# Optimization experiments

Hardware: AMD Instinct MI355X
Metric: run time of the kernel (lower is better)

Reference implementation:

```python
import jax, jax.numpy as jnp
import numpy as np

B = 8192
DIMS = [1024, 1024, 1024, 1024]  # input, hidden0, hidden1, output
RANK = 64


def _apg_layer(x, Wm, bm, U, V, b, activate):
    # hyper-net (MLP_Layer with no hidden units == single Linear): generates rank*rank weights per sample
    w = (x @ Wm.T + bm).reshape(x.shape[0], RANK, RANK)   # [B, r, r]
    u = x @ U.T                                           # U_matrix: [B, r]
    # (u.unsqueeze(-1) * w).sum(-2) == per-sample matvec
    h = jnp.einsum('br,brs->bs', u, w)                    # [B, r]
    out = h @ V.T + b                                     # V_matrix + static bias: [B, out]
    return jax.nn.relu(out) if activate else out


def setup_inputs() -> dict:
    key = jax.random.key(0)
    ks = jax.random.split(key, 16)
    inp = {"x": jax.random.normal(ks[0], (B, DIMS[0]), dtype=jnp.float32)}
    ki = 1
    for l in range(3):
        din, dout = DIMS[l], DIMS[l + 1]
        inp[f"Wm{l}"] = jax.random.normal(ks[ki], (RANK * RANK, din), dtype=jnp.float32) * (1.0 / np.sqrt(din)); ki += 1
        inp[f"bm{l}"] = jnp.zeros((RANK * RANK,), dtype=jnp.float32)
        inp[f"U{l}"] = jax.random.normal(ks[ki], (RANK, din), dtype=jnp.float32) * (1.0 / np.sqrt(din)); ki += 1
        inp[f"V{l}"] = jax.random.normal(ks[ki], (dout, RANK), dtype=jnp.float32) * (1.0 / np.sqrt(RANK)); ki += 1
        inp[f"b{l}"] = jnp.zeros((dout,), dtype=jnp.float32)
    return inp


def reference(x, Wm0, bm0, U0, V0, b0, Wm1, bm1, U1, V1, b1, Wm2, bm2, U2, V2, b2):
    h = _apg_layer(x, Wm0, bm0, U0, V0, b0, activate=True)   # hidden layer 0 + ReLU
    h = _apg_layer(h, Wm1, bm1, U1, V1, b1, activate=True)   # hidden layer 1 + ReLU
    out = _apg_layer(h, Wm2, bm2, U2, V2, b2, activate=False)  # output layer, no activation
    return out
```

## Files before the change

### kernel.cpp

```cpp
#include <hip/hip_runtime.h>
#include <stdint.h>

typedef short bf16x8_t __attribute__((ext_vector_type(8)));
typedef short bf16x4_t __attribute__((ext_vector_type(4)));
typedef float f32x4_t __attribute__((ext_vector_type(4)));
typedef unsigned short u16x4_t __attribute__((ext_vector_type(4)));
typedef unsigned short u16x8_t __attribute__((ext_vector_type(8)));

#define DEV static __device__ __forceinline__

DEV float bf2f(unsigned short u) {
  union { unsigned int i; float f; } v; v.i = ((unsigned int)u) << 16; return v.f;
}
DEV unsigned short f2bf(float f) {
  union { float f; unsigned int i; } v; v.f = f;
  unsigned int x = v.i;
  unsigned int lsb = (x >> 16) & 1u;
  x += 0x7fffu + lsb;
  return (unsigned short)(x >> 16);
}

struct CvtSeg {
  const float* src[3];
  unsigned short* dst[3];
  int bstart[4];
};

DEV void cvt_block(const CvtSeg& cs, int vb, int tid) {
  int seg = (vb >= cs.bstart[1] ? 1 : 0) + (vb >= cs.bstart[2] ? 1 : 0);
  int local = (vb - cs.bstart[seg]) * 256 + tid;
  float4 v = ((const float4*)cs.src[seg])[local];
  u16x4_t o = { f2bf(v.x), f2bf(v.y), f2bf(v.z), f2bf(v.w) };
  *(u16x4_t*)&cs.dst[seg][local * 4] = o;
}

__global__ __launch_bounds__(256) void k_cvt(CvtSeg cs) {
  cvt_block(cs, blockIdx.x, threadIdx.x);
}

__global__ __launch_bounds__(256, 2) void xu_fused(
    const float* __restrict__ x,
    const unsigned short* __restrict__ U0,
    unsigned short* __restrict__ xb,
    unsigned short* __restrict__ u_out) {
  __shared__ unsigned short tlds[4 * 16 * 72];
  __shared__ float upart[4 * 16 * 68];

  const int tid = threadIdx.x;
  const int lane = tid & 63;
  const int w = tid >> 6;
  const int fr = lane & 15;
  const int quad = lane >> 4;
  const int rowBase = blockIdx.x * 16;

  unsigned short* tl = &tlds[w * 16 * 72];
  const int m2 = lane >> 2;
  const int kc = (lane & 3) * 16;

  f32x4_t uacc[4];
#pragma unroll
  for (int n = 0; n < 4; n++) uacc[n] = f32x4_t{0.f, 0.f, 0.f, 0.f};

  for (int it = 0; it < 4; ++it) {
    const int cb = w * 256 + it * 64;

    {
      const float* xp = x + (size_t)(rowBase + m2) * 1024 + cb + kc;
      float4 v0 = *(const float4*)(xp);
      float4 v1 = *(const float4*)(xp + 4);
      float4 v2 = *(const float4*)(xp + 8);
      float4 v3 = *(const float4*)(xp + 12);
      u16x8_t o0 = { f2bf(v0.x), f2bf(v0.y), f2bf(v0.z), f2bf(v0.w),
                     f2bf(v1.x), f2bf(v1.y), f2bf(v1.z), f2bf(v1.w) };
      u16x8_t o1 = { f2bf(v2.x), f2bf(v2.y), f2bf(v2.z), f2bf(v2.w),
                     f2bf(v3.x), f2bf(v3.y), f2bf(v3.z), f2bf(v3.w) };
      *(u16x8_t*)&tl[m2 * 72 + kc] = o0;
      *(u16x8_t*)&tl[m2 * 72 + kc + 8] = o1;
      unsigned short* xo = xb + (size_t)(rowBase + m2) * 1024 + cb + kc;
      *(u16x8_t*)xo = o0;
      *(u16x8_t*)(xo + 8) = o1;
    }

#pragma unroll
    for (int ks = 0; ks < 2; ++ks) {
      bf16x8_t at = *(const bf16x8_t*)&tl[fr * 72 + ks * 32 + quad * 8];
#pragma unroll
      for (int n = 0; n < 4; n++) {
        bf16x8_t bu = *(const bf16x8_t*)&U0[(size_t)(n * 16 + fr) * 1024 + cb +
                                            ks * 32 + quad * 8];
        uacc[n] = __builtin_amdgcn_mfma_f32_16x16x32_bf16(at, bu, uacc[n], 0, 0, 0);
      }
    }
  }

  {
    float* up = &upart[w * 16 * 68];
#pragma unroll
    for (int n = 0; n < 4; n++)
#pragma unroll
      for (int r = 0; r < 4; r++)
        up[(quad * 4 + r) * 68 + n * 16 + fr] = uacc[n][r];
  }
  __syncthreads();
  {
    int m = tid >> 4;
    int c0 = (tid & 15) * 4;
    f32x4_t s = {0.f, 0.f, 0.f, 0.f};
#pragma unroll
    for (int wv = 0; wv < 4; wv++)
      s += *(const f32x4_t*)&upart[wv * 16 * 68 + m * 68 + c0];
    u16x4_t o = { f2bf(s[0]), f2bf(s[1]), f2bf(s[2]), f2bf(s[3]) };
    *(u16x4_t*)&u_out[(size_t)(rowBase + m) * 64 + c0] = o;
  }
}

__global__ __launch_bounds__(256, 2) void k_hyper(
    const unsigned short* __restrict__ A,
    const unsigned short* __restrict__ Wmb,
    const unsigned short* __restrict__ ug,
    const float* __restrict__ bm,
    unsigned short* __restrict__ h_out,
    CvtSeg cs) {
  __shared__ unsigned short smem[16384];

  if (blockIdx.x >= 2048) {
    cvt_block(cs, blockIdx.x - 2048, threadIdx.x);
    return;
  }

  unsigned short* As = smem;
  unsigned short* Bs = smem + 8192;
  const int K = 1024;

  const int tid = threadIdx.x;
  const int lane = tid & 63;
  const int w = tid >> 6;
  const int wrow0 = (w & 1) * 64;
  const int wcol0 = (w >> 1) * 64;
  const int bx = blockIdx.x & 31;
  const int by = blockIdx.x >> 5;
  const int rowBase = by * 128;
  const int colBase = bx * 128;

  const int rl = lane >> 3;
  const int kbg = (lane & 7) ^ rl;
  const int fr = lane & 15;
  const int quad = lane >> 4;

  f32x4_t acc[4][4];
#pragma unroll
  for (int i = 0; i < 4; i++)
#pragma unroll
    for (int j = 0; j < 4; j++) acc[i][j] = f32x4_t{0.f, 0.f, 0.f, 0.f};

  for (int kt = 0; kt < K; kt += 64) {
    __syncthreads();
#pragma unroll
    for (int jj = 0; jj < 4; ++jj) {
      int tr = w * 32 + jj * 8 + rl;
      int ct = colBase + tr;
      int pr = ((ct & 63) << 6) | (ct >> 6);
      const unsigned short* ga = A + (size_t)(rowBase + tr) * K + kt + kbg * 8;
      const unsigned short* gb = Wmb + (size_t)pr * K + kt + kbg * 8;
      __builtin_amdgcn_global_load_lds(
          (const __attribute__((address_space(1))) void*)ga,
          (__attribute__((address_space(3))) void*)&As[(w * 32 + jj * 8) * 64],
          16, 0, 0);
      __builtin_amdgcn_global_load_lds(
          (const __attribute__((address_space(1))) void*)gb,
          (__attribute__((address_space(3))) void*)&Bs[(w * 32 + jj * 8) * 64],
          16, 0, 0);
    }
    __syncthreads();

#pragma unroll
    for (int ks = 0; ks < 2; ++ks) {
      bf16x8_t a[4], b[4];
#pragma unroll
      for (int i = 0; i < 4; i++) {
        int m = wrow0 + i * 16 + fr;
        int slot = (ks * 4 + quad) ^ (m & 7);
        a[i] = *(const bf16x8_t*)&As[m * 64 + slot * 8];
      }
#pragma unroll
      for (int j = 0; j < 4; j++) {
        int n = wcol0 + j * 16 + fr;
        int slot = (ks * 4 + quad) ^ (n & 7);
        b[j] = *(const bf16x8_t*)&Bs[n * 64 + slot * 8];
      }
#pragma unroll
      for (int i = 0; i < 4; i++)
#pragma unroll
        for (int j = 0; j < 4; j++)
          acc[i][j] = __builtin_amdgcn_mfma_f32_16x16x32_bf16(a[i], b[j],
                                                              acc[i][j], 0, 0, 0);
    }
  }

  __syncthreads();

  {
    int row = tid >> 1;
    int c0 = (tid & 1) * 32;
    const unsigned short* up = ug + (size_t)(rowBase + row) * 64 + c0;
    bf16x8_t v0 = *(const bf16x8_t*)(up);
    bf16x8_t v1 = *(const bf16x8_t*)(up + 8);
    bf16x8_t v2 = *(const bf16x8_t*)(up + 16);
    bf16x8_t v3 = *(const bf16x8_t*)(up + 24);
#pragma unroll
    for (int m = 0; m < 8; m++) {
      smem[(c0 + m) * 136 + row] = (unsigned short)v0[m];
      smem[(c0 + 8 + m) * 136 + row] = (unsigned short)v1[m];
      smem[(c0 + 16 + m) * 136 + row] = (unsigned short)v2[m];
      smem[(c0 + 24 + m) * 136 + row] = (unsigned short)v3[m];
    }
  }
  __syncthreads();

  const int s = bx * 2 + (w >> 1);
  float bmv[4];
#pragma unroll
  for (int j = 0; j < 4; j++) bmv[j] = bm[(j * 16 + fr) * 64 + s];

#pragma unroll
  for (int i = 0; i < 4; i++) {
    int row0 = wrow0 + i * 16 + quad * 4;
    bf16x4_t uv[4];
#pragma unroll
    for (int j = 0; j < 4; j++)
      uv[j] = *(const bf16x4_t*)&smem[(j * 16 + fr) * 136 + row0];
#pragma unroll
    for (int r = 0; r < 4; r++) {
      float p = 0.f;
#pragma unroll
      for (int j = 0; j < 4; j++)
        p += bf2f((unsigned short)uv[j][r]) * (acc[i][j][r] + bmv[j]);
      p += __shfl_xor(p, 1, 64);
      p += __shfl_xor(p, 2, 64);
      p += __shfl_xor(p, 4, 64);
      p += __shfl_xor(p, 8, 64);
      if (fr == 0)
        h_out[(size_t)(rowBase + row0 + r) * 64 + s] = f2bf(p);
    }
  }
}

__global__ __launch_bounds__(256, 2) void vu_fused(
    const unsigned short* __restrict__ h,
    const unsigned short* __restrict__ Vb,
    const float* __restrict__ bias,
    const unsigned short* __restrict__ Un,
    unsigned short* __restrict__ act,
    unsigned short* __restrict__ u_out) {
  __shared__ unsigned short tlds[4 * 16 * 72];
  __shared__ float upart[4 * 16 * 68];

  const int tid = threadIdx.x;
  const int lane = tid & 63;
  const int w = tid >> 6;
  const int fr = lane & 15;
  const int quad = lane >> 4;
  const int rowBase = blockIdx.x * 16;

  unsigned short* tl = &tlds[w * 16 * 72];

  bf16x8_t ah0 = *(const bf16x8_t*)&h[(size_t)(rowBase + fr) * 64 + quad * 8];
  bf16x8_t ah1 = *(const bf16x8_t*)&h[(size_t)(rowBase + fr) * 64 + 32 + quad * 8];

  f32x4_t uacc[4];
#pragma unroll
  for (int n = 0; n < 4; n++) uacc[n] = f32x4_t{0.f, 0.f, 0.f, 0.f};

  for (int it = 0; it < 4; ++it) {
    const int cb = w * 256 + it * 64;

    f32x4_t tacc[4];
#pragma unroll
    for (int nt = 0; nt < 4; nt++) {
      const unsigned short* vrow = Vb + (size_t)(cb + nt * 16 + fr) * 64;
      bf16x8_t b0 = *(const bf16x8_t*)&vrow[quad * 8];
      bf16x8_t b1 = *(const bf16x8_t*)&vrow[32 + quad * 8];
      f32x4_t z = {0.f, 0.f, 0.f, 0.f};
      z = __builtin_amdgcn_mfma_f32_16x16x32_bf16(ah0, b0, z, 0, 0, 0);
      tacc[nt] = __builtin_amdgcn_mfma_f32_16x16x32_bf16(ah1, b1, z, 0, 0, 0);
    }

#pragma unroll
    for (int nt = 0; nt < 4; nt++) {
      float bv = bias[cb + nt * 16 + fr];
#pragma unroll
      for (int r = 0; r < 4; r++) {
        float v = tacc[nt][r] + bv;
        v = v > 0.f ? v : 0.f;
        tl[(quad * 4 + r) * 72 + nt * 16 + fr] = f2bf(v);
      }
    }

    {
      int m2 = lane >> 2;
      int kc = (lane & 3) * 16;
      bf16x8_t t0 = *(const bf16x8_t*)&tl[m2 * 72 + kc];
      bf16x8_t t1 = *(const bf16x8_t*)&tl[m2 * 72 + kc + 8];
      unsigned short* ap = act + (size_t)(rowBase + m2) * 1024 + cb + kc;
      *(bf16x8_t*)ap = t0;
      *(bf16x8_t*)(ap + 8) = t1;
    }

#pragma unroll
    for (int ks = 0; ks < 2; ++ks) {
      bf16x8_t at = *(const bf16x8_t*)&tl[fr * 72 + ks * 32 + quad * 8];
#pragma unroll
      for (int n = 0; n < 4; n++) {
        bf16x8_t bu = *(const bf16x8_t*)&Un[(size_t)(n * 16 + fr) * 1024 + cb +
                                            ks * 32 + quad * 8];
        uacc[n] = __builtin_amdgcn_mfma_f32_16x16x32_bf16(at, bu, uacc[n], 0, 0, 0);
      }
    }
  }

  {
    float* up = &upart[w * 16 * 68];
#pragma unroll
    for (int n = 0; n < 4; n++)
#pragma unroll
      for (int r = 0; r < 4; r++)
        up[(quad * 4 + r) * 68 + n * 16 + fr] = uacc[n][r];
  }
  __syncthreads();
  {
    int m = tid >> 4;
    int c0 = (tid & 15) * 4;
    f32x4_t s = {0.f, 0.f, 0.f, 0.f};
#pragma unroll
    for (int wv = 0; wv < 4; wv++)
      s += *(const f32x4_t*)&upart[wv * 16 * 68 + m * 68 + c0];
    u16x4_t o = { f2bf(s[0]), f2bf(s[1]), f2bf(s[2]), f2bf(s[3]) };
    *(u16x4_t*)&u_out[(size_t)(rowBase + m) * 64 + c0] = o;
  }
}

__global__ __launch_bounds__(256, 2) void k_final(
    const unsigned short* __restrict__ A, const unsigned short* __restrict__ B,
    const float* __restrict__ bias, float* __restrict__ Cout) {
  __shared__ unsigned short As[128 * 64];
  __shared__ unsigned short Bs[128 * 64];

  const int tid = threadIdx.x;
  const int lane = tid & 63;
  const int w = tid >> 6;
  const int wrow0 = (w & 1) * 64;
  const int wcol0 = (w >> 1) * 64;
  const int rowBase = blockIdx.y * 128;
  const int colBase = blockIdx.x * 128;

  const int rl = lane >> 3;
  const int kbg = (lane & 7) ^ rl;
  const int fr = lane & 15;
  const int quad = lane >> 4;

  f32x4_t acc[4][4];
#pragma unroll
  for (int i = 0; i < 4; i++)
#pragma unroll
    for (int j = 0; j < 4; j++) acc[i][j] = f32x4_t{0.f, 0.f, 0.f, 0.f};

  __syncthreads();
#pragma unroll
  for (int jj = 0; jj < 4; ++jj) {
    int tr = w * 32 + jj * 8 + rl;
    const unsigned short* ga = A + (size_t)(rowBase + tr) * 64 + kbg * 8;
    const unsigned short* gb = B + (size_t)(colBase + tr) * 64 + kbg * 8;
    __builtin_amdgcn_global_load_lds(
        (const __attribute__((address_space(1))) void*)ga,
        (__attribute__((address_space(3))) void*)&As[(w * 32 + jj * 8) * 64],
        16, 0, 0);
    __builtin_amdgcn_global_load_lds(
        (const __attribute__((address_space(1))) void*)gb,
        (__attribute__((address_space(3))) void*)&Bs[(w * 32 + jj * 8) * 64],
        16, 0, 0);
  }
  __syncthreads();

#pragma unroll
  for (int ks = 0; ks < 2; ++ks) {
    bf16x8_t a[4], b[4];
#pragma unroll
    for (int i = 0; i < 4; i++) {
      int m = wrow0 + i * 16 + fr;
      int slot = (ks * 4 + quad) ^ (m & 7);
      a[i] = *(const bf16x8_t*)&As[m * 64 + slot * 8];
    }
#pragma unroll
    for (int j = 0; j < 4; j++) {
      int n = wcol0 + j * 16 + fr;
      int slot = (ks * 4 + quad) ^ (n & 7);
      b[j] = *(const bf16x8_t*)&Bs[n * 64 + slot * 8];
    }
#pragma unroll
    for (int i = 0; i < 4; i++)
#pragma unroll
      for (int j = 0; j < 4; j++)
        acc[i][j] = __builtin_amdgcn_mfma_f32_16x16x32_bf16(a[i], b[j],
                                                            acc[i][j], 0, 0, 0);
  }

#pragma unroll
  for (int j = 0; j < 4; j++) {
    int col = colBase + wcol0 + j * 16 + fr;
    float bv = bias[col];
#pragma unroll
    for (int i = 0; i < 4; i++) {
#pragma unroll
      for (int r = 0; r < 4; r++) {
        int row = rowBase + wrow0 + i * 16 + quad * 4 + r;
        Cout[(size_t)row * 1024 + col] = acc[i][j][r] + bv;
      }
    }
  }
}

extern "C" void kernel_launch(void* const* d_in, const int* in_sizes, int n_in,
                              void* d_out, int out_size, void* d_ws,
                              size_t ws_size, hipStream_t stream) {
  const float* x = (const float*)d_in[0];
  const float* Wm[3] = {(const float*)d_in[1], (const float*)d_in[6], (const float*)d_in[11]};
  const float* bm[3] = {(const float*)d_in[2], (const float*)d_in[7], (const float*)d_in[12]};
  const float* U[3]  = {(const float*)d_in[3], (const float*)d_in[8], (const float*)d_in[13]};
  const float* V[3]  = {(const float*)d_in[4], (const float*)d_in[9], (const float*)d_in[14]};
  const float* bs[3] = {(const float*)d_in[5], (const float*)d_in[10], (const float*)d_in[15]};

  char* p = (char*)d_ws;
  unsigned short* xb = (unsigned short*)p;  p += 8192UL * 1024 * 2;
  unsigned short* act = (unsigned short*)p; p += 8192UL * 1024 * 2;
  unsigned short* Wmb[3];
  for (int l = 0; l < 3; l++) { Wmb[l] = (unsigned short*)p; p += 4096UL * 1024 * 2; }
  unsigned short* Ub[3];
  for (int l = 0; l < 3; l++) { Ub[l] = (unsigned short*)p; p += 64UL * 1024 * 2; }
  unsigned short* Vb[3];
  for (int l = 0; l < 3; l++) { Vb[l] = (unsigned short*)p; p += 1024UL * 64 * 2; }
  unsigned short* hb = (unsigned short*)p;  p += 8192UL * 64 * 2;
  unsigned short* ug = (unsigned short*)p;  p += 8192UL * 64 * 2;

  CvtSeg c0;
  c0.src[0] = Wm[0]; c0.dst[0] = Wmb[0];
  c0.src[1] = U[0];  c0.dst[1] = Ub[0];
  c0.src[2] = U[0];  c0.dst[2] = Ub[0];
  c0.bstart[0] = 0; c0.bstart[1] = 4096; c0.bstart[2] = 4160; c0.bstart[3] = 4160;
  k_cvt<<<4160, 256, 0, stream>>>(c0);

  xu_fused<<<512, 256, 0, stream>>>(x, Ub[0], xb, ug);

  CvtSeg ch[3];
  ch[0].src[0] = Wm[1]; ch[0].dst[0] = Wmb[1];
  ch[0].src[1] = U[1];  ch[0].dst[1] = Ub[1];
  ch[0].src[2] = V[0];  ch[0].dst[2] = Vb[0];
  ch[0].bstart[0] = 0; ch[0].bstart[1] = 4096; ch[0].bstart[2] = 4160; ch[0].bstart[3] = 4224;
  ch[1].src[0] = Wm[2]; ch[1].dst[0] = Wmb[2];
  ch[1].src[1] = U[2];  ch[1].dst[1] = Ub[2];
  ch[1].src[2] = V[1];  ch[1].dst[2] = Vb[1];
  ch[1].bstart[0] = 0; ch[1].bstart[1] = 4096; ch[1].bstart[2] = 4160; ch[1].bstart[3] = 4224;
  ch[2].src[0] = V[2]; ch[2].dst[0] = Vb[2];
  ch[2].src[1] = V[2]; ch[2].dst[1] = Vb[2];
  ch[2].src[2] = V[2]; ch[2].dst[2] = Vb[2];
  ch[2].bstart[0] = 0; ch[2].bstart[1] = 64; ch[2].bstart[2] = 64; ch[2].bstart[3] = 64;

  const int hyperGrid[3] = {2048 + 4224, 2048 + 4224, 2048 + 64};

  const unsigned short* cur = xb;
  for (int l = 0; l < 3; l++) {
    k_hyper<<<hyperGrid[l], 256, 0, stream>>>(cur, Wmb[l], ug, bm[l], hb, ch[l]);
    if (l < 2) {
      vu_fused<<<512, 256, 0, stream>>>(hb, Vb[l], bs[l], Ub[l + 1], act, ug);
      cur = act;
    } else {
      k_final<<<dim3(8, 64), 256, 0, stream>>>(hb, Vb[2], bs[2], (float*)d_out);
    }
  }
}
```

Before: 413.8 us.

## Rewrite hyper GEMM with 256x256 tiles, 8 waves, 4-stage LDS pipeline

The hypernetwork GEMM kernel moves from 128x128 tiles with 4 waves and single-buffered K=64 steps to 256x256 tiles with 8 waves (512 threads). It uses a 4-slot ring of K=32 LDS buffers filled by direct global-to-LDS loads issued two steps ahead, with explicit waitcnt, barriers and s_setprio around the MFMA bursts. The aim is to hide global load latency and raise data reuse per tile. The cost is 128KB of LDS per block and far fewer blocks (512), which limits occupancy. The fused conversion blocks are resized to 512 threads to match.

```diff
diff --git a/kernel.cpp b/kernel.cpp
--- a/kernel.cpp
+++ b/kernel.cpp
@@ -29,6 +29,14 @@
 DEV void cvt_block(const CvtSeg& cs, int vb, int tid) {
   int seg = (vb >= cs.bstart[1] ? 1 : 0) + (vb >= cs.bstart[2] ? 1 : 0);
   int local = (vb - cs.bstart[seg]) * 256 + tid;
+  float4 v = ((const float4*)cs.src[seg])[local];
+  u16x4_t o = { f2bf(v.x), f2bf(v.y), f2bf(v.z), f2bf(v.w) };
+  *(u16x4_t*)&cs.dst[seg][local * 4] = o;
+}
+
+DEV void cvt_block512(const CvtSeg& cs, int vb, int tid) {
+  int seg = (vb >= cs.bstart[1] ? 1 : 0) + (vb >= cs.bstart[2] ? 1 : 0);
+  int local = (vb - cs.bstart[seg]) * 512 + tid;
   float4 v = ((const float4*)cs.src[seg])[local];
   u16x4_t o = { f2bf(v.x), f2bf(v.y), f2bf(v.z), f2bf(v.w) };
   *(u16x4_t*)&cs.dst[seg][local * 4] = o;
@@ -114,87 +122,113 @@
   }
 }
 
-__global__ __launch_bounds__(256, 2) void k_hyper(
+#define GLD(gp, lp)                                              \
+  __builtin_amdgcn_global_load_lds(                              \
+      (const __attribute__((address_space(1))) void*)(gp),       \
+      (__attribute__((address_space(3))) void*)(lp), 16, 0, 0)
+
+__global__ __launch_bounds__(512, 2) void k_hyper(
     const unsigned short* __restrict__ A,
     const unsigned short* __restrict__ Wmb,
     const unsigned short* __restrict__ ug,
     const float* __restrict__ bm,
     unsigned short* __restrict__ h_out,
     CvtSeg cs) {
-  __shared__ unsigned short smem[16384];
-
-  if (blockIdx.x >= 2048) {
-    cvt_block(cs, blockIdx.x - 2048, threadIdx.x);
+  __shared__ unsigned short lds[65536];
+
+  if (blockIdx.x >= 512) {
+    cvt_block512(cs, blockIdx.x - 512, threadIdx.x);
     return;
   }
 
-  unsigned short* As = smem;
-  unsigned short* Bs = smem + 8192;
-  const int K = 1024;
+  unsigned short* As = lds;
+  unsigned short* Bs = lds + 32768;
 
   const int tid = threadIdx.x;
   const int lane = tid & 63;
   const int w = tid >> 6;
-  const int wrow0 = (w & 1) * 64;
-  const int wcol0 = (w >> 1) * 64;
-  const int bx = blockIdx.x & 31;
-  const int by = blockIdx.x >> 5;
-  const int rowBase = by * 128;
-  const int colBase = bx * 128;
-
-  const int rl = lane >> 3;
-  const int kbg = (lane & 7) ^ rl;
+  const int wr = w >> 2;
+  const int wc = w & 3;
+  const int bx = blockIdx.x & 15;
+  const int by = blockIdx.x >> 4;
+  const int rowBase = by * 256;
+  const int colBase = bx * 256;
   const int fr = lane & 15;
   const int quad = lane >> 4;
 
-  f32x4_t acc[4][4];
-#pragma unroll
-  for (int i = 0; i < 4; i++)
+  const int lrow = lane >> 2;
+  const int lchunk = (lane & 3) ^ (lrow & 3);
+  const int tr0 = w * 16 + lrow;
+  const int tr1 = 128 + w * 16 + lrow;
+  const unsigned short* gA0 = A + (size_t)(rowBase + tr0) * 1024 + lchunk * 8;
+  const unsigned short* gA1 = A + (size_t)(rowBase + tr1) * 1024 + lchunk * 8;
+  const int ct0 = colBase + tr0;
+  const int ct1 = colBase + tr1;
+  const unsigned short* gB0 =
+      Wmb + (size_t)(((ct0 & 63) << 6) | (ct0 >> 6)) * 1024 + lchunk * 8;
+  const unsigned short* gB1 =
+      Wmb + (size_t)(((ct1 & 63) << 6) | (ct1 >> 6)) * 1024 + lchunk * 8;
+  const int dst0 = w * 512;
+  const int dst1 = 4096 + w * 512;
+
+  const int aoff = (wr * 128 + fr) * 32 + ((quad ^ (fr & 3)) * 8);
+  const int boff = (wc * 64 + fr) * 32 + ((quad ^ (fr & 3)) * 8);
+
+  f32x4_t acc[8][4];
+#pragma unroll
+  for (int i = 0; i < 8; i++)
 #pragma unroll
     for (int j = 0; j < 4; j++) acc[i][j] = f32x4_t{0.f, 0.f, 0.f, 0.f};
 
-  for (int kt = 0; kt < K; kt += 64) {
-    __syncthreads();
-#pragma unroll
-    for (int jj = 0; jj < 4; ++jj) {
-      int tr = w * 32 + jj * 8 + rl;
-      int ct = colBase + tr;
-      int pr = ((ct & 63) << 6) | (ct >> 6);
-      const unsigned short* ga = A + (size_t)(rowBase + tr) * K + kt + kbg * 8;
-      const unsigned short* gb = Wmb + (size_t)pr * K + kt + kbg * 8;
-      __builtin_amdgcn_global_load_lds(
-          (const __attribute__((address_space(1))) void*)ga,
-          (__attribute__((address_space(3))) void*)&As[(w * 32 + jj * 8) * 64],
-          16, 0, 0);
-      __builtin_amdgcn_global_load_lds(
-          (const __attribute__((address_space(1))) void*)gb,
-          (__attribute__((address_space(3))) void*)&Bs[(w * 32 + jj * 8) * 64],
-          16, 0, 0);
-    }
-    __syncthreads();
-
-#pragma unroll
-    for (int ks = 0; ks < 2; ++ks) {
-      bf16x8_t a[4], b[4];
-#pragma unroll
-      for (int i = 0; i < 4; i++) {
-        int m = wrow0 + i * 16 + fr;
-        int slot = (ks * 4 + quad) ^ (m & 7);
-        a[i] = *(const bf16x8_t*)&As[m * 64 + slot * 8];
-      }
-#pragma unroll
-      for (int j = 0; j < 4; j++) {
-        int n = wcol0 + j * 16 + fr;
-        int slot = (ks * 4 + quad) ^ (n & 7);
-        b[j] = *(const bf16x8_t*)&Bs[n * 64 + slot * 8];
-      }
-#pragma unroll
-      for (int i = 0; i < 4; i++)
-#pragma unroll
-        for (int j = 0; j < 4; j++)
-          acc[i][j] = __builtin_amdgcn_mfma_f32_16x16x32_bf16(a[i], b[j],
-                                                              acc[i][j], 0, 0, 0);
-    }
+#define STAGE_A(t) do { int sl_ = (t) & 3;                  \
+    GLD(gA0 + (t) * 32, &As[sl_ * 8192 + dst0]);            \
+    GLD(gA1 + (t) * 32, &As[sl_ * 8192 + dst1]); } while (0)
+#define STAGE_B(t) do { int sl_ = (t) & 3;                  \
+    GLD(gB0 + (t) * 32, &Bs[sl_ * 8192 + dst0]);            \
+    GLD(gB1 + (t) * 32, &Bs[sl_ * 8192 + dst1]); } while (0)
+
+  STAGE_A(0); STAGE_B(0); STAGE_A(1); STAGE_B(1);
+  asm volatile("s_waitcnt vmcnt(4)" ::: "memory");
+  __builtin_amdgcn_s_barrier();
+
+  for (int t = 0; t < 32; ++t) {
+    const unsigned short* Asl = &As[(t & 3) * 8192];
+    const unsigned short* Bsl = &Bs[(t & 3) * 8192];
+    bf16x8_t a0[4], b[4];
+#pragma unroll
+    for (int i = 0; i < 4; i++) a0[i] = *(const bf16x8_t*)&Asl[aoff + i * 512];
+#pragma unroll
+    for (int n = 0; n < 4; n++) b[n] = *(const bf16x8_t*)&Bsl[boff + n * 512];
+    if (t < 30) STAGE_A(t + 2);
+    __builtin_amdgcn_s_barrier();
+    asm volatile("s_waitcnt lgkmcnt(0)" ::: "memory");
+    __builtin_amdgcn_s_setprio(1);
+#pragma unroll
+    for (int i = 0; i < 4; i++)
+#pragma unroll
+      for (int n = 0; n < 4; n++)
+        acc[i][n] =
+            __builtin_amdgcn_mfma_f32_16x16x32_bf16(a0[i], b[n], acc[i][n], 0, 0, 0);
+    __builtin_amdgcn_s_setprio(0);
+    __builtin_amdgcn_s_barrier();
+    bf16x8_t a1[4];
+#pragma unroll
+    for (int i = 0; i < 4; i++)
+      a1[i] = *(const bf16x8_t*)&Asl[aoff + (i + 4) * 512];
+    if (t < 30) STAGE_B(t + 2);
+    __builtin_amdgcn_s_barrier();
+    asm volatile("s_waitcnt lgkmcnt(0)" ::: "memory");
+    __builtin_amdgcn_s_setprio(1);
+#pragma unroll
+    for (int i = 0; i < 4; i++)
+#pragma unroll
+      for (int n = 0; n < 4; n++)
+        acc[i + 4][n] = __builtin_amdgcn_mfma_f32_16x16x32_bf16(a1[i], b[n],
+                                                                acc[i + 4][n], 0, 0, 0);
+    __builtin_amdgcn_s_setprio(0);
+    if (t < 30) { asm volatile("s_waitcnt vmcnt(4)" ::: "memory"); }
+    else        { asm volatile("s_waitcnt vmcnt(0)" ::: "memory"); }
+    __builtin_amdgcn_s_barrier();
   }
 
   __syncthreads();
@@ -209,26 +243,26 @@
     bf16x8_t v3 = *(const bf16x8_t*)(up + 24);
 #pragma unroll
     for (int m = 0; m < 8; m++) {
-      smem[(c0 + m) * 136 + row] = (unsigned short)v0[m];
-      smem[(c0 + 8 + m) * 136 + row] = (unsigned short)v1[m];
-      smem[(c0 + 16 + m) * 136 + row] = (unsigned short)v2[m];
-      smem[(c0 + 24 + m) * 136 + row] = (unsigned short)v3[m];
+      lds[(c0 + m) * 264 + row] = (unsigned short)v0[m];
+      lds[(c0 + 8 + m) * 264 + row] = (unsigned short)v1[m];
+      lds[(c0 + 16 + m) * 264 + row] = (unsigned short)v2[m];
+      lds[(c0 + 24 + m) * 264 + row] = (unsigned short)v3[m];
     }
   }
   __syncthreads();
 
-  const int s = bx * 2 + (w >> 1);
+  const int s = bx * 4 + wc;
   float bmv[4];
 #pragma unroll
   for (int j = 0; j < 4; j++) bmv[j] = bm[(j * 16 + fr) * 64 + s];
 
 #pragma unroll
-  for (int i = 0; i < 4; i++) {
-    int row0 = wrow0 + i * 16 + quad * 4;
+  for (int i = 0; i < 8; i++) {
+    int row0 = wr * 128 + i * 16 + quad * 4;
     bf16x4_t uv[4];
 #pragma unroll
     for (int j = 0; j < 4; j++)
-      uv[j] = *(const bf16x4_t*)&smem[(j * 16 + fr) * 136 + row0];
+      uv[j] = *(const bf16x4_t*)&lds[(j * 16 + fr) * 264 + row0];
 #pragma unroll
     for (int r = 0; r < 4; r++) {
       float p = 0.f;
@@ -454,21 +488,21 @@
   ch[0].src[0] = Wm[1]; ch[0].dst[0] = Wmb[1];
   ch[0].src[1] = U[1];  ch[0].dst[1] = Ub[1];
   ch[0].src[2] = V[0];  ch[0].dst[2] = Vb[0];
-  ch[0].bstart[0] = 0; ch[0].bstart[1] = 4096; ch[0].bstart[2] = 4160; ch[0].bstart[3] = 4224;
+  ch[0].bstart[0] = 0; ch[0].bstart[1] = 2048; ch[0].bstart[2] = 2080; ch[0].bstart[3] = 2112;
   ch[1].src[0] = Wm[2]; ch[1].dst[0] = Wmb[2];
   ch[1].src[1] = U[2];  ch[1].dst[1] = Ub[2];
   ch[1].src[2] = V[1];  ch[1].dst[2] = Vb[1];
-  ch[1].bstart[0] = 0; ch[1].bstart[1] = 4096; ch[1].bstart[2] = 4160; ch[1].bstart[3] = 4224;
+  ch[1].bstart[0] = 0; ch[1].bstart[1] = 2048; ch[1].bstart[2] = 2080; ch[1].bstart[3] = 2112;
   ch[2].src[0] = V[2]; ch[2].dst[0] = Vb[2];
   ch[2].src[1] = V[2]; ch[2].dst[1] = Vb[2];
   ch[2].src[2] = V[2]; ch[2].dst[2] = Vb[2];
-  ch[2].bstart[0] = 0; ch[2].bstart[1] = 64; ch[2].bstart[2] = 64; ch[2].bstart[3] = 64;
-
-  const int hyperGrid[3] = {2048 + 4224, 2048 + 4224, 2048 + 64};
+  ch[2].bstart[0] = 0; ch[2].bstart[1] = 32; ch[2].bstart[2] = 32; ch[2].bstart[3] = 32;
+
+  const int hyperGrid[3] = {512 + 2112, 512 + 2112, 512 + 32};
 
   const unsigned short* cur = xb;
   for (int l = 0; l < 3; l++) {
-    k_hyper<<<hyperGrid[l], 256, 0, stream>>>(cur, Wmb[l], ug, bm[l], hb, ch[l]);
+    k_hyper<<<hyperGrid[l], 512, 0, stream>>>(cur, Wmb[l], ug, bm[l], hb, ch[l]);
     if (l < 2) {
       vu_fused<<<512, 256, 0, stream>>>(hb, Vb[l], bs[l], Ub[l + 1], act, ug);
       cur = act;
```

Measured after the change: 437.0 us. 1.06x slower.
